# Performance work log

Measured on AMD Instinct MI355X. Metric: run time of the kernel, lower is better.

## Reference

```python
import jax, jax.numpy as jnp
import numpy as np

EMBED_DIM = 1024
NUM_HEADS = 8
SEQ_LEN = 2048
EPS = 1e-6


def setup_inputs() -> dict:
    key = jax.random.key(0)
    ks = jax.random.split(key, 8)
    E, NH, S = EMBED_DIM, NUM_HEADS, SEQ_LEN
    q = jax.random.normal(ks[0], (S, E), jnp.float32)
    k = jax.random.normal(ks[1], (S, E), jnp.float32)
    v = jax.random.normal(ks[2], (S, E), jnp.float32)
    # gate projections: weights init'd to zeros in the module; use small random
    # values so the gate math is exercised. Biases follow the module's init.
    Wi = 0.02 * jax.random.normal(ks[3], (NH, 3 * E), jnp.float32)
    bi = jnp.linspace(3.0, 6.0, NH, dtype=jnp.float32)
    Wf = 0.02 * jax.random.normal(ks[4], (NH, 3 * E), jnp.float32)
    bf = jnp.sqrt(0.1) * jax.random.normal(ks[5], (NH,), jnp.float32)
    # ResidualLayerNorm (xLSTM-style): effective scale = 1 + weight, no bias
    ln_weight = jnp.zeros((E,), jnp.float32)
    return {"q": q, "k": k, "v": v, "Wi": Wi, "bi": bi, "Wf": Wf, "bf": bf,
            "ln_weight": ln_weight}


def _mlstm_parallel(q, k, v, Wi, bi, Wf, bf, ln_weight):
    S, E = q.shape
    NH = Wi.shape[0]
    DH = E // NH
    gate_in = jnp.concatenate((q, k, v), axis=1)            # (S, 3E)
    ig = (gate_in @ Wi.T + bi).T[:, :, None]                # (NH, S, 1)
    fg = (gate_in @ Wf.T + bf).T[:, :, None]                # (NH, S, 1)

    qh = q.reshape(S, NH, DH).transpose(1, 0, 2)            # (NH, S, DH)
    kh = k.reshape(S, NH, DH).transpose(1, 0, 2)
    vh = v.reshape(S, NH, DH).transpose(1, 0, 2)

    # cumulative log forget gates
    log_f = jax.nn.log_sigmoid(fg)                          # (NH, S, 1)
    log_f_cum = jnp.concatenate(
        [jnp.zeros((NH, 1, 1), q.dtype), jnp.cumsum(log_f, axis=1)], axis=1
    )                                                       # (NH, S+1, 1)
    log_fg_mat = log_f_cum - log_f_cum.transpose(0, 2, 1)   # (NH, S+1, S+1)
    causal = jnp.tril(jnp.ones((S, S), bool))
    log_fg_mat = jnp.where(causal, log_fg_mat[:, 1:, 1:], -jnp.inf)  # (NH,S,S)

    log_D = log_fg_mat + ig.transpose(0, 2, 1)              # (NH, S, S)
    max_log_D = jnp.max(log_D, axis=-1, keepdims=True)      # (NH, S, 1)
    D = jnp.exp(log_D - max_log_D)                          # stabilized

    qk = jnp.einsum('hsd,htd->hst', qh, kh) / jnp.sqrt(jnp.asarray(DH, q.dtype))
    C = qk * D                                              # (NH, S, S)
    normalizer = jnp.maximum(jnp.abs(jnp.sum(C, axis=-1, keepdims=True)),
                             jnp.exp(-max_log_D))
    C_norm = C / (normalizer + EPS)
    h = jnp.einsum('hst,htd->hsd', C_norm, vh)              # (NH, S, DH)
    h = h.transpose(1, 0, 2).reshape(S, E)

    # residual layer norm: LN(h) * (1 + weight), no bias
    mu = jnp.mean(h, axis=-1, keepdims=True)
    var = jnp.mean(jnp.square(h - mu), axis=-1, keepdims=True)
    h_norm = (h - mu) * jax.lax.rsqrt(var + 1e-5)
    return h_norm * (1.0 + ln_weight)


def reference(q, k, v, Wi, bi, Wf, bf, ln_weight):
    return _mlstm_parallel(q, k, v, Wi, bi, Wf, bf, ln_weight)
```

## Files before the change

### kernel.cpp

```cpp
#include <hip/hip_runtime.h>
#include <math.h>

#define S_LEN 2048
#define EMB   1024
#define NHEAD 8
#define DH    128
#define E3    3072
#define BM    64
#define BN    32
#define NSPLIT 4
#define KSPLIT 8
#define KCH   (E3 / KSPLIT)
#define NGEMM (32 * KSPLIT)
#define PTSTRIDE 40

typedef __bf16 bf16x8 __attribute__((ext_vector_type(8)));
typedef __bf16 bf16x4 __attribute__((ext_vector_type(4)));
typedef float  f32x4  __attribute__((ext_vector_type(4)));

__device__ __forceinline__ void gload16(const __bf16* g, __bf16* l) {
    __builtin_amdgcn_global_load_lds(
        (const __attribute__((address_space(1))) void*)g,
        (__attribute__((address_space(3))) void*)l, 16, 0, 0);
}

__global__ __launch_bounds__(256) void gates_gemm_cvt_trans_kernel(
    const float* __restrict__ q, const float* __restrict__ k,
    const float* __restrict__ v,
    const float* __restrict__ Wi, const float* __restrict__ Wf,
    __bf16* __restrict__ Qh, __bf16* __restrict__ Ql,
    __bf16* __restrict__ Kh, __bf16* __restrict__ Kl,
    __bf16* __restrict__ Vt, float* __restrict__ gpart)
{
    const int tid = threadIdx.x;
    const int bid = blockIdx.x;
    __shared__ __bf16 tile[32][33];

    if (bid < NGEMM) {
        const int tt = bid >> 3, ks = bid & (KSPLIT - 1);
        const int w = tid >> 6, lane = tid & 63;
        const int quad = lane >> 4, l15 = lane & 15;
        const int tbase = tt * 64 + w * 16;
        const float* wrow = (l15 < 8) ? (Wi + l15 * E3) : (Wf + (l15 - 8) * E3);
        f32x4 acc = {0.f, 0.f, 0.f, 0.f};
        #pragma unroll
        for (int j = 0; j < KCH / 32; ++j) {
            const int K0 = ks * KCH + j * 32;
            const float* src; int off;
            if (K0 < 1024)      { src = q; off = K0; }
            else if (K0 < 2048) { src = k; off = K0 - 1024; }
            else                { src = v; off = K0 - 2048; }
            const float* ap = src + (size_t)(tbase + l15) * EMB + off + quad * 8;
            float4 a0 = *(const float4*)ap,       a1 = *(const float4*)(ap + 4);
            const float* bp = wrow + K0 + quad * 8;
            float4 b0 = *(const float4*)bp,       b1 = *(const float4*)(bp + 4);
            float af[8] = {a0.x,a0.y,a0.z,a0.w,a1.x,a1.y,a1.z,a1.w};
            float bfv[8] = {b0.x,b0.y,b0.z,b0.w,b1.x,b1.y,b1.z,b1.w};
            bf16x8 ah, al, bh, bl;
            #pragma unroll
            for (int e = 0; e < 8; ++e) {
                __bf16 ha = (__bf16)af[e];
                ah[e] = ha; al[e] = (__bf16)(af[e] - (float)ha);
                __bf16 hb = (__bf16)bfv[e];
                bh[e] = hb; bl[e] = (__bf16)(bfv[e] - (float)hb);
            }
            acc = __builtin_amdgcn_mfma_f32_16x16x32_bf16(ah, bh, acc, 0, 0, 0);
            acc = __builtin_amdgcn_mfma_f32_16x16x32_bf16(ah, bl, acc, 0, 0, 0);
            acc = __builtin_amdgcn_mfma_f32_16x16x32_bf16(al, bh, acc, 0, 0, 0);
        }
        float* gp = gpart + (size_t)(ks * 16 + l15) * S_LEN + tbase;
        #pragma unroll
        for (int r = 0; r < 4; ++r) gp[quad * 4 + r] = acc[r];
    } else if (bid < NGEMM + S_LEN) {
        const int t = bid - NGEMM;
        const float4 qv = ((const float4*)q)[(size_t)t * 256 + tid];
        const float4 kv = ((const float4*)k)[(size_t)t * 256 + tid];
        size_t idx = (size_t)t * 256 + tid;
        bf16x4 hi, lo;
        hi[0]=(__bf16)qv.x; hi[1]=(__bf16)qv.y; hi[2]=(__bf16)qv.z; hi[3]=(__bf16)qv.w;
        lo[0]=(__bf16)(qv.x-(float)hi[0]); lo[1]=(__bf16)(qv.y-(float)hi[1]);
        lo[2]=(__bf16)(qv.z-(float)hi[2]); lo[3]=(__bf16)(qv.w-(float)hi[3]);
        ((bf16x4*)Qh)[idx] = hi; ((bf16x4*)Ql)[idx] = lo;
        hi[0]=(__bf16)kv.x; hi[1]=(__bf16)kv.y; hi[2]=(__bf16)kv.z; hi[3]=(__bf16)kv.w;
        lo[0]=(__bf16)(kv.x-(float)hi[0]); lo[1]=(__bf16)(kv.y-(float)hi[1]);
        lo[2]=(__bf16)(kv.z-(float)hi[2]); lo[3]=(__bf16)(kv.w-(float)hi[3]);
        ((bf16x4*)Kh)[idx] = hi; ((bf16x4*)Kl)[idx] = lo;
    } else {
        const int tb = bid - NGEMM - S_LEN;
        const int sb = (tb & 63) * 32, eb = (tb >> 6) * 32;
        #pragma unroll
        for (int i = 0; i < 4; ++i) {
            int lin = tid + i * 256;
            int sr = lin >> 5, ec = lin & 31;
            tile[ec][sr] = (__bf16)v[(size_t)(sb + sr) * EMB + eb + ec];
        }
        __syncthreads();
        #pragma unroll
        for (int i = 0; i < 4; ++i) {
            int lin = tid + i * 256;
            int er = lin >> 5, sc = lin & 31;
            Vt[(size_t)(eb + er) * S_LEN + sb + sc] = tile[er][sc];
        }
    }
}

__global__ __launch_bounds__(256) void cumsum_aux_kernel(
    const float* __restrict__ gpart,
    const float* __restrict__ bi, const float* __restrict__ bfp,
    float* __restrict__ F, float* __restrict__ ug,
    float* __restrict__ umax, float* __restrict__ upmax)
{
    const int h = blockIdx.x, tid = threadIdx.x;
    const int lane = tid & 63, w = tid >> 6;
    __shared__ float wsum[4];
    __shared__ float morig[256];
    const float bih = bi[h], bfh = bfp[h];
    float loc[8], igv[8];
    const int base = tid * 8;
    float s = 0.f;
    for (int i = 0; i < 8; i++) {
        const int t = base + i;
        float ri = 0.f, rf = 0.f;
        #pragma unroll
        for (int ks = 0; ks < KSPLIT; ++ks) {
            ri += gpart[(size_t)(ks * 16 + h) * S_LEN + t];
            rf += gpart[(size_t)(ks * 16 + 8 + h) * S_LEN + t];
        }
        igv[i] = ri + bih;
        float x = rf + bfh;
        float lfv = fminf(x, 0.f) - log1pf(expf(-fabsf(x)));
        s += lfv; loc[i] = s;
    }
    float inc = s;
    #pragma unroll
    for (int o = 1; o < 64; o <<= 1) {
        float t = __shfl_up(inc, o, 64);
        if (lane >= o) inc += t;
    }
    if (lane == 63) wsum[w] = inc;
    __syncthreads();
    float wpre = 0.f;
    #pragma unroll
    for (int i = 0; i < 4; ++i) if (i < w) wpre += wsum[i];
    const float prev = wpre + inc - s;
    float* Fh = F + h * (S_LEN + 1);
    if (tid == 0) Fh[0] = 0.f;
    float Fv[8];
    for (int i = 0; i < 8; i++) { Fv[i] = prev + loc[i]; Fh[base + i + 1] = Fv[i]; }

    float pm[8];
    float runm = -1e30f;
    #pragma unroll
    for (int i = 0; i < 8; i++) {
        float u = igv[i] - Fv[i];
        ug[h * S_LEN + base + i] = u;
        runm = fmaxf(runm, u);
        pm[i] = runm;
    }
    morig[tid] = runm;
    __syncthreads();
    const int g0 = tid & ~3;
    float pfx = -1e30f;
    for (int j = g0; j < tid; ++j) pfx = fmaxf(pfx, morig[j]);
    #pragma unroll
    for (int i = 0; i < 8; i++)
        upmax[h * S_LEN + base + i] = fmaxf(pfx, pm[i]);
    if ((tid & 3) == 0) {
        float mm = fmaxf(fmaxf(morig[tid], morig[tid + 1]),
                         fmaxf(morig[tid + 2], morig[tid + 3]));
        umax[h * 64 + (tid >> 2)] = mm;
    }
}

__global__ __launch_bounds__(256, 2) void mlstm_mfma(
    const __bf16* __restrict__ Qhg, const __bf16* __restrict__ Qlg,
    const __bf16* __restrict__ Khg, const __bf16* __restrict__ Klg,
    const __bf16* __restrict__ Vtg,
    const float* __restrict__ ug, const float* __restrict__ umaxg,
    const float* __restrict__ upmaxg, const float* __restrict__ F,
    __bf16* __restrict__ Opart, float* __restrict__ msplit,
    float* __restrict__ lsplit)
{
    const int flat = blockIdx.x;
    const int h = flat & 7;
    const int rest = flat >> 3;
    const int xx = rest & 15, z = rest >> 4;
    const int tid  = threadIdx.x;
    const int lane = tid & 63, w = tid >> 6;
    const int quad = lane >> 4, l15 = lane & 15;

    __shared__ __bf16 KhL[2][4096];
    __shared__ __bf16 KlL[2][4096];
    __shared__ __bf16 VtL[4096];
    __shared__ __bf16 Pt[4][16 * PTSTRIDE];

    const float* Fh  = F  + h * (S_LEN + 1);
    const float* ugh = ug + h * S_LEN;
    const float scale = 0.088388347648318447f;

    const int krow0 = tid >> 4;
    const int krow1 = 16 + krow0;
    const int kchk  = (tid & 15) ^ (krow0 & 15);
    const int vrow0 = tid >> 2;
    const int vrow1 = 64 + vrow0;
    const int vchk  = (tid & 3) ^ ((vrow0 ^ (vrow0 >> 2)) & 3);
    const int ldsw  = w * 512;

#define STAGE_K(B, TB) do {                                                   \
    const __bf16* kb_ = Khg + (size_t)(TB) * EMB + h * DH;                    \
    const __bf16* lb_ = Klg + (size_t)(TB) * EMB + h * DH;                    \
    gload16(kb_ + (size_t)krow0 * EMB + kchk * 8, &KhL[B][ldsw]);             \
    gload16(kb_ + (size_t)krow1 * EMB + kchk * 8, &KhL[B][2048 + ldsw]);      \
    gload16(lb_ + (size_t)krow0 * EMB + kchk * 8, &KlL[B][ldsw]);             \
    gload16(lb_ + (size_t)krow1 * EMB + kchk * 8, &KlL[B][2048 + ldsw]);      \
} while (0)
#define STAGE_V(TB) do {                                                      \
    const __bf16* vg_ = Vtg + (size_t)(h * DH) * S_LEN + (TB);                \
    gload16(vg_ + (size_t)vrow0 * S_LEN + vchk * 8, &VtL[ldsw]);              \
    gload16(vg_ + (size_t)vrow1 * S_LEN + vchk * 8, &VtL[2048 + ldsw]);       \
} while (0)

    for (int pair = 0; pair < 2; ++pair) {
        const int qt = (pair == 0) ? xx : 31 - xx;
        const int qb = qt * BM;
        const int nj = 2 * qt + 2;
        const int j0 = (z * nj) / NSPLIT, j1 = ((z + 1) * nj) / NSPLIT;
        const int qbw = qb + w * 16;
        const int SBLK = (qb >> 5) + (w >> 1);

        float fq[4], upm[4];
        int sglob[4];
        #pragma unroll
        for (int r = 0; r < 4; ++r) {
            int s = qbw + quad * 4 + r;
            sglob[r] = s;
            fq[r]  = Fh[s + 1];
            upm[r] = upmaxg[h * S_LEN + s];
        }

        bf16x8 qh[4], ql[4];
        {
            const size_t qrow = (size_t)(qbw + l15) * EMB + h * DH + quad * 8;
            #pragma unroll
            for (int kk = 0; kk < 4; ++kk) {
                qh[kk] = *(const bf16x8*)(Qhg + qrow + kk * 32);
                ql[kk] = *(const bf16x8*)(Qlg + qrow + kk * 32);
            }
        }
        #pragma unroll
        for (int kk = 0; kk < 4; ++kk)
            asm volatile("" : "+v"(qh[kk]), "+v"(ql[kk]));

        float m_r[4] = {-1e30f, -1e30f, -1e30f, -1e30f};
        float l_r[4] = {0.f, 0.f, 0.f, 0.f};
        f32x4 Oacc[8] = {{0,0,0,0},{0,0,0,0},{0,0,0,0},{0,0,0,0},
                         {0,0,0,0},{0,0,0,0},{0,0,0,0},{0,0,0,0}};

        float pu0 = 0.f, pu1 = 0.f, pum = 0.f;
        int buf = 0;
        if (j0 < j1) {
            STAGE_K(0, j0 * BN);
            pu0 = ugh[j0 * BN + l15];
            pu1 = ugh[j0 * BN + 16 + l15];
            pum = umaxg[h * 64 + j0];
            __syncthreads();
        }

        for (int j = j0; j < j1; ++j) {
            const int tb = j * BN;
            STAGE_V(tb);
            if (j + 1 < j1) STAGE_K(buf ^ 1, tb + BN);
            const float ut0 = pu0, ut1 = pu1, umj = pum;
            if (j + 1 < j1) {
                pu0 = ugh[tb + BN + l15];
                pu1 = ugh[tb + BN + 16 + l15];
                pum = umaxg[h * 64 + (j + 1)];
            }
            if (j <= SBLK) {
                f32x4 S0 = {0,0,0,0}, S1 = {0,0,0,0};
                #pragma unroll
                for (int kk = 0; kk < 4; ++kk) {
                    const int kpos = (((kk << 2) | quad) ^ l15) * 8;
                    bf16x8 bh0 = *(const bf16x8*)&KhL[buf][l15 * 128 + kpos];
                    bf16x8 bl0 = *(const bf16x8*)&KlL[buf][l15 * 128 + kpos];
                    S0 = __builtin_amdgcn_mfma_f32_16x16x32_bf16(qh[kk], bh0, S0, 0, 0, 0);
                    S0 = __builtin_amdgcn_mfma_f32_16x16x32_bf16(qh[kk], bl0, S0, 0, 0, 0);
                    S0 = __builtin_amdgcn_mfma_f32_16x16x32_bf16(ql[kk], bh0, S0, 0, 0, 0);
                    bf16x8 bh1 = *(const bf16x8*)&KhL[buf][(16 + l15) * 128 + kpos];
                    bf16x8 bl1 = *(const bf16x8*)&KlL[buf][(16 + l15) * 128 + kpos];
                    S1 = __builtin_amdgcn_mfma_f32_16x16x32_bf16(qh[kk], bh1, S1, 0, 0, 0);
                    S1 = __builtin_amdgcn_mfma_f32_16x16x32_bf16(qh[kk], bl1, S1, 0, 0, 0);
                    S1 = __builtin_amdgcn_mfma_f32_16x16x32_bf16(ql[kk], bh1, S1, 0, 0, 0);
                }
                const int t0 = tb + l15, t1 = tb + 16 + l15;
                #pragma unroll
                for (int r = 0; r < 4; ++r) {
                    float mt = (j < SBLK) ? (fq[r] + umj) : (fq[r] + upm[r]);
                    float mn = fmaxf(m_r[r], mt);
                    float alpha = __expf(m_r[r] - mn);
                    m_r[r] = mn;
                    #pragma unroll
                    for (int nt = 0; nt < 8; ++nt) Oacc[nt][r] *= alpha;
                    float p0 = __expf(fq[r] + ut0 - mn) * S0[r] * scale;
                    float p1 = __expf(fq[r] + ut1 - mn) * S1[r] * scale;
                    if (j == SBLK) {
                        if (t0 > sglob[r]) p0 = 0.f;
                        if (t1 > sglob[r]) p1 = 0.f;
                    }
                    l_r[r] = l_r[r] * alpha + (p0 + p1);
                    const int prow = (quad * 4 + r) * PTSTRIDE;
                    Pt[w][prow + l15]      = (__bf16)p0;
                    Pt[w][prow + 16 + l15] = (__bf16)p1;
                }
            }
            __syncthreads();
            if (j <= SBLK) {
                bf16x8 pa = *(const bf16x8*)&Pt[w][l15 * PTSTRIDE + quad * 8];
                #pragma unroll
                for (int nt = 0; nt < 8; ++nt) {
                    const int vrow = nt * 16 + l15;
                    const int vpos = (quad ^ ((vrow ^ (vrow >> 2)) & 3)) * 8;
                    bf16x8 vv = *(const bf16x8*)&VtL[vrow * 32 + vpos];
                    Oacc[nt] = __builtin_amdgcn_mfma_f32_16x16x32_bf16(pa, vv, Oacc[nt], 0, 0, 0);
                }
            }
            __syncthreads();
            buf ^= 1;
        }
        __bf16* Oz = Opart + (size_t)z * S_LEN * EMB;
        #pragma unroll
        for (int nt = 0; nt < 8; ++nt) {
            #pragma unroll
            for (int r = 0; r < 4; ++r) {
                Oz[(size_t)sglob[r] * EMB + h * DH + nt * 16 + l15] = (__bf16)Oacc[nt][r];
            }
        }
        #pragma unroll
        for (int r = 0; r < 4; ++r) {
            float x = l_r[r];
            #pragma unroll
            for (int o = 1; o < 16; o <<= 1) x += __shfl_xor(x, o);
            l_r[r] = x;
        }
        if (l15 == 0) {
            #pragma unroll
            for (int r = 0; r < 4; ++r) {
                msplit[(z * NHEAD + h) * S_LEN + sglob[r]] = m_r[r];
                lsplit[(z * NHEAD + h) * S_LEN + sglob[r]] = l_r[r];
            }
        }
    }
#undef STAGE_K
#undef STAGE_V
}

__global__ __launch_bounds__(256) void combine_ln_kernel(
    const __bf16* __restrict__ Opart, const float* __restrict__ msplit,
    const float* __restrict__ lsplit, const float* __restrict__ lnw,
    float* __restrict__ out)
{
    const int tid = threadIdx.x;
    const int r  = tid >> 7;
    const int wr = (tid >> 6) & 1;
    const int c0 = (tid & 127) * 8;
    const int hh = c0 >> 7;
    const int s  = blockIdx.x * 2 + r;
    __shared__ float redsum[2][2], redvar[2][2];

    float m = -1e30f, es[NSPLIT], l = 0.f;
    #pragma unroll
    for (int zz = 0; zz < NSPLIT; ++zz)
        m = fmaxf(m, msplit[(zz * NHEAD + hh) * S_LEN + s]);
    #pragma unroll
    for (int zz = 0; zz < NSPLIT; ++zz) {
        es[zz] = __expf(msplit[(zz * NHEAD + hh) * S_LEN + s] - m);
        l += es[zz] * lsplit[(zz * NHEAD + hh) * S_LEN + s];
    }
    const float rn = 1.f / (fmaxf(fabsf(l), __expf(-m)) + 1e-6f);

    const size_t SE = (size_t)S_LEN * EMB;
    float x[8] = {0,0,0,0,0,0,0,0};
    #pragma unroll
    for (int zz = 0; zz < NSPLIT; ++zz) {
        if (es[zz] != 0.f) {
            bf16x8 o = *(const bf16x8*)(Opart + zz * SE + (size_t)s * EMB + c0);
            #pragma unroll
            for (int e = 0; e < 8; ++e) x[e] += es[zz] * (float)o[e];
        }
    }
    float sum = 0.f;
    #pragma unroll
    for (int e = 0; e < 8; ++e) { x[e] *= rn; sum += x[e]; }
    for (int o = 32; o > 0; o >>= 1) sum += __shfl_down(sum, o, 64);
    if ((tid & 63) == 0) redsum[r][wr] = sum;
    __syncthreads();
    sum = redsum[r][0] + redsum[r][1];
    const float mu = sum * (1.f / EMB);
    float vs = 0.f;
    #pragma unroll
    for (int e = 0; e < 8; ++e) { float d = x[e] - mu; vs += d * d; }
    for (int o = 32; o > 0; o >>= 1) vs += __shfl_down(vs, o, 64);
    if ((tid & 63) == 0) redvar[r][wr] = vs;
    __syncthreads();
    vs = redvar[r][0] + redvar[r][1];
    const float rstd = rsqrtf(vs * (1.f / EMB) + 1e-5f);
    const float4 w0 = *(const float4*)(lnw + c0);
    const float4 w1 = *(const float4*)(lnw + c0 + 4);
    float4 o0, o1;
    o0.x = (x[0]-mu)*rstd*(1.f+w0.x); o0.y = (x[1]-mu)*rstd*(1.f+w0.y);
    o0.z = (x[2]-mu)*rstd*(1.f+w0.z); o0.w = (x[3]-mu)*rstd*(1.f+w0.w);
    o1.x = (x[4]-mu)*rstd*(1.f+w1.x); o1.y = (x[5]-mu)*rstd*(1.f+w1.y);
    o1.z = (x[6]-mu)*rstd*(1.f+w1.z); o1.w = (x[7]-mu)*rstd*(1.f+w1.w);
    *(float4*)(out + (size_t)s * EMB + c0)     = o0;
    *(float4*)(out + (size_t)s * EMB + c0 + 4) = o1;
}

extern "C" void kernel_launch(void* const* d_in, const int* in_sizes, int n_in,
                              void* d_out, int out_size, void* d_ws, size_t ws_size,
                              hipStream_t stream)
{
    const float* q   = (const float*)d_in[0];
    const float* k   = (const float*)d_in[1];
    const float* v   = (const float*)d_in[2];
    const float* Wi  = (const float*)d_in[3];
    const float* bi  = (const float*)d_in[4];
    const float* Wf  = (const float*)d_in[5];
    const float* bf  = (const float*)d_in[6];
    const float* lnw = (const float*)d_in[7];
    float* out = (float*)d_out;

    float* ws = (float*)d_ws;
    float* gpart = ws;
    float* F     = gpart + KSPLIT * 16 * S_LEN;
    float* ugw   = F + NHEAD * (S_LEN + 1);
    float* umaxw = ugw + NHEAD * S_LEN;
    float* upmaxw= umaxw + NHEAD * 64;
    __bf16* Qh = (__bf16*)(upmaxw + NHEAD * S_LEN);
    const size_t SEb = (size_t)S_LEN * EMB;
    __bf16* Ql  = Qh + SEb;
    __bf16* Kh  = Ql + SEb;
    __bf16* Kl  = Kh + SEb;
    __bf16* Vtg = Kl + SEb;
    __bf16* Opart = Vtg + SEb;
    float* msplit = (float*)(Opart + (size_t)NSPLIT * SEb);
    float* lsplit = msplit + NSPLIT * NHEAD * S_LEN;

    gates_gemm_cvt_trans_kernel<<<NGEMM + S_LEN + 2048, 256, 0, stream>>>(
        q, k, v, Wi, Wf, Qh, Ql, Kh, Kl, Vtg, gpart);
    cumsum_aux_kernel<<<NHEAD, 256, 0, stream>>>(
        gpart, bi, bf, F, ugw, umaxw, upmaxw);
    mlstm_mfma<<<16 * NHEAD * NSPLIT, 256, 0, stream>>>(
        Qh, Ql, Kh, Kl, Vtg, ugw, umaxw, upmaxw, F, Opart, msplit, lsplit);
    combine_ln_kernel<<<S_LEN / 2, 256, 0, stream>>>(Opart, msplit, lsplit, lnw, out);
}
```

Before: 147.4 us.

## Fuse Q bf16 split into attention kernel and raise KV split count

Removes the Q hi/lo bf16 conversion from the preprocessing kernel. The attention kernel now loads fp32 Q directly and splits it in registers, which saves writing and re-reading two bf16 Q arrays. NSPLIT goes from 4 to 6, giving 768 attention blocks instead of 512 for better CU occupancy. Blocks with no work skip their Opart stores. The trade-offs are more partial outputs for the combine kernel to merge and redundant Q conversion in each split block. Because Opart writes can now be skipped, correctness depends on the combine kernel handling empty splits through their m/l values.

```diff
diff --git a/kernel.cpp b/kernel.cpp
--- a/kernel.cpp
+++ b/kernel.cpp
@@ -8,7 +8,7 @@
 #define E3    3072
 #define BM    64
 #define BN    32
-#define NSPLIT 4
+#define NSPLIT 6
 #define KSPLIT 8
 #define KCH   (E3 / KSPLIT)
 #define NGEMM (32 * KSPLIT)
@@ -28,7 +28,6 @@
     const float* __restrict__ q, const float* __restrict__ k,
     const float* __restrict__ v,
     const float* __restrict__ Wi, const float* __restrict__ Wf,
-    __bf16* __restrict__ Qh, __bf16* __restrict__ Ql,
     __bf16* __restrict__ Kh, __bf16* __restrict__ Kl,
     __bf16* __restrict__ Vt, float* __restrict__ gpart)
 {
@@ -73,14 +72,9 @@
         for (int r = 0; r < 4; ++r) gp[quad * 4 + r] = acc[r];
     } else if (bid < NGEMM + S_LEN) {
         const int t = bid - NGEMM;
-        const float4 qv = ((const float4*)q)[(size_t)t * 256 + tid];
         const float4 kv = ((const float4*)k)[(size_t)t * 256 + tid];
         size_t idx = (size_t)t * 256 + tid;
         bf16x4 hi, lo;
-        hi[0]=(__bf16)qv.x; hi[1]=(__bf16)qv.y; hi[2]=(__bf16)qv.z; hi[3]=(__bf16)qv.w;
-        lo[0]=(__bf16)(qv.x-(float)hi[0]); lo[1]=(__bf16)(qv.y-(float)hi[1]);
-        lo[2]=(__bf16)(qv.z-(float)hi[2]); lo[3]=(__bf16)(qv.w-(float)hi[3]);
-        ((bf16x4*)Qh)[idx] = hi; ((bf16x4*)Ql)[idx] = lo;
         hi[0]=(__bf16)kv.x; hi[1]=(__bf16)kv.y; hi[2]=(__bf16)kv.z; hi[3]=(__bf16)kv.w;
         lo[0]=(__bf16)(kv.x-(float)hi[0]); lo[1]=(__bf16)(kv.y-(float)hi[1]);
         lo[2]=(__bf16)(kv.z-(float)hi[2]); lo[3]=(__bf16)(kv.w-(float)hi[3]);
@@ -173,7 +167,7 @@
 }
 
 __global__ __launch_bounds__(256, 2) void mlstm_mfma(
-    const __bf16* __restrict__ Qhg, const __bf16* __restrict__ Qlg,
+    const float* __restrict__ Qg,
     const __bf16* __restrict__ Khg, const __bf16* __restrict__ Klg,
     const __bf16* __restrict__ Vtg,
     const float* __restrict__ ug, const float* __restrict__ umaxg,
@@ -238,24 +232,6 @@
             upm[r] = upmaxg[h * S_LEN + s];
         }
 
-        bf16x8 qh[4], ql[4];
-        {
-            const size_t qrow = (size_t)(qbw + l15) * EMB + h * DH + quad * 8;
-            #pragma unroll
-            for (int kk = 0; kk < 4; ++kk) {
-                qh[kk] = *(const bf16x8*)(Qhg + qrow + kk * 32);
-                ql[kk] = *(const bf16x8*)(Qlg + qrow + kk * 32);
-            }
-        }
-        #pragma unroll
-        for (int kk = 0; kk < 4; ++kk)
-            asm volatile("" : "+v"(qh[kk]), "+v"(ql[kk]));
-
-        float m_r[4] = {-1e30f, -1e30f, -1e30f, -1e30f};
-        float l_r[4] = {0.f, 0.f, 0.f, 0.f};
-        f32x4 Oacc[8] = {{0,0,0,0},{0,0,0,0},{0,0,0,0},{0,0,0,0},
-                         {0,0,0,0},{0,0,0,0},{0,0,0,0},{0,0,0,0}};
-
         float pu0 = 0.f, pu1 = 0.f, pum = 0.f;
         int buf = 0;
         if (j0 < j1) {
@@ -263,8 +239,34 @@
             pu0 = ugh[j0 * BN + l15];
             pu1 = ugh[j0 * BN + 16 + l15];
             pum = umaxg[h * 64 + j0];
-            __syncthreads();
-        }
+        }
+
+        bf16x8 qh[4], ql[4];
+        {
+            const float* qp = Qg + (size_t)(qbw + l15) * EMB + h * DH + quad * 8;
+            #pragma unroll
+            for (int kk = 0; kk < 4; ++kk) {
+                float4 a = *(const float4*)(qp + kk * 32);
+                float4 b = *(const float4*)(qp + kk * 32 + 4);
+                float f[8] = {a.x, a.y, a.z, a.w, b.x, b.y, b.z, b.w};
+                #pragma unroll
+                for (int e = 0; e < 8; ++e) {
+                    __bf16 hi = (__bf16)f[e];
+                    qh[kk][e] = hi;
+                    ql[kk][e] = (__bf16)(f[e] - (float)hi);
+                }
+            }
+        }
+        #pragma unroll
+        for (int kk = 0; kk < 4; ++kk)
+            asm volatile("" : "+v"(qh[kk]), "+v"(ql[kk]));
+
+        float m_r[4] = {-1e30f, -1e30f, -1e30f, -1e30f};
+        float l_r[4] = {0.f, 0.f, 0.f, 0.f};
+        f32x4 Oacc[8] = {{0,0,0,0},{0,0,0,0},{0,0,0,0},{0,0,0,0},
+                         {0,0,0,0},{0,0,0,0},{0,0,0,0},{0,0,0,0}};
+
+        if (j0 < j1) __syncthreads();
 
         for (int j = j0; j < j1; ++j) {
             const int tb = j * BN;
@@ -327,12 +329,15 @@
             __syncthreads();
             buf ^= 1;
         }
-        __bf16* Oz = Opart + (size_t)z * S_LEN * EMB;
-        #pragma unroll
-        for (int nt = 0; nt < 8; ++nt) {
-            #pragma unroll
-            for (int r = 0; r < 4; ++r) {
-                Oz[(size_t)sglob[r] * EMB + h * DH + nt * 16 + l15] = (__bf16)Oacc[nt][r];
+        const bool active = (j0 < j1) && (j0 <= SBLK);
+        if (active) {
+            __bf16* Oz = Opart + (size_t)z * S_LEN * EMB;
+            #pragma unroll
+            for (int nt = 0; nt < 8; ++nt) {
+                #pragma unroll
+                for (int r = 0; r < 4; ++r) {
+                    Oz[(size_t)sglob[r] * EMB + h * DH + nt * 16 + l15] = (__bf16)Oacc[nt][r];
+                }
             }
         }
         #pragma unroll
@@ -435,10 +440,8 @@
     float* ugw   = F + NHEAD * (S_LEN + 1);
     float* umaxw = ugw + NHEAD * S_LEN;
     float* upmaxw= umaxw + NHEAD * 64;
-    __bf16* Qh = (__bf16*)(upmaxw + NHEAD * S_LEN);
+    __bf16* Kh = (__bf16*)(upmaxw + NHEAD * S_LEN);
     const size_t SEb = (size_t)S_LEN * EMB;
-    __bf16* Ql  = Qh + SEb;
-    __bf16* Kh  = Ql + SEb;
     __bf16* Kl  = Kh + SEb;
     __bf16* Vtg = Kl + SEb;
     __bf16* Opart = Vtg + SEb;
@@ -446,10 +449,10 @@
     float* lsplit = msplit + NSPLIT * NHEAD * S_LEN;
 
     gates_gemm_cvt_trans_kernel<<<NGEMM + S_LEN + 2048, 256, 0, stream>>>(
-        q, k, v, Wi, Wf, Qh, Ql, Kh, Kl, Vtg, gpart);
+        q, k, v, Wi, Wf, Kh, Kl, Vtg, gpart);
     cumsum_aux_kernel<<<NHEAD, 256, 0, stream>>>(
         gpart, bi, bf, F, ugw, umaxw, upmaxw);
     mlstm_mfma<<<16 * NHEAD * NSPLIT, 256, 0, stream>>>(
-        Qh, Ql, Kh, Kl, Vtg, ugw, umaxw, upmaxw, F, Opart, msplit, lsplit);
+        q, Kh, Kl, Vtg, ugw, umaxw, upmaxw, F, Opart, msplit, lsplit);
     combine_ln_kernel<<<S_LEN / 2, 256, 0, stream>>>(Opart, msplit, lsplit, lnw, out);
 }
```

New measurement: 149.6 us. No clear change (+1.5%).
